# Optimization experiments

Measured on AMD Instinct MI355X. Metric: run time of the kernel, lower is better.

The kernel has to match this reference:

```python
import jax, jax.numpy as jnp
import numpy as np

V, H, L, B, T = 128, 1024, 2, 64, 512

def setup_inputs() -> dict:
    key = jax.random.key(0)
    ks = jax.random.split(key, 6)
    idx = jax.random.randint(ks[0], (B, T), 0, V, dtype=jnp.int32)
    embed = jax.random.normal(ks[1], (V, H), dtype=jnp.float32) * 0.02
    Wx = jax.random.normal(ks[2], (L, H, 4 * H), dtype=jnp.float32) * (1.0 / np.sqrt(H))
    Wh = jax.random.normal(ks[3], (L, H, 4 * H), dtype=jnp.float32) * (1.0 / np.sqrt(H))
    b = jnp.zeros((L, 4 * H), dtype=jnp.float32)
    W_out = jax.random.normal(ks[4], (H, V), dtype=jnp.float32) * (1.0 / np.sqrt(H))
    return {"idx": idx, "embed": embed, "Wx": Wx, "Wh": Wh, "b": b, "W_out": W_out}

def reference(idx, embed, Wx, Wh, b, W_out):
    # idx: (B,T) int32; embed: (V,H); Wx,Wh: (L,H,4H); b: (L,4H); W_out: (H,V)
    x = embed[idx]                      # (B,T,H)
    Bv, Tv, Hv = x.shape
    Lv = Wx.shape[0]
    c0 = jnp.zeros((Lv, Bv, Hv), dtype=x.dtype)
    h0 = jnp.zeros((Lv, Bv, Hv), dtype=x.dtype)

    def step(carry, x_t):
        c, h = carry                    # each (L,B,H)
        new_c, new_h = [], []
        h_in = x_t                      # (B,H)
        for i in range(Lv):             # fixed small layer count
            gates = h_in @ Wx[i] + h[i] @ Wh[i] + b[i]   # (B,4H)
            i_g, f_g, g_g, o_g = jnp.split(gates, 4, axis=-1)
            c_new = jax.nn.sigmoid(f_g) * c[i] + jax.nn.sigmoid(i_g) * jnp.tanh(g_g)
            h_new = jax.nn.sigmoid(o_g) * jnp.tanh(c_new)
            new_c.append(c_new)
            new_h.append(h_new)
            h_in = h_new                # eval mode: dropout mask == 1
        return (jnp.stack(new_c), jnp.stack(new_h)), h_in

    _, hs_tm = jax.lax.scan(step, (c0, h0), jnp.swapaxes(x, 0, 1))  # (T,B,H)
    hs = jnp.swapaxes(hs_tm, 0, 1)                                  # (B,T,H)
    return hs @ W_out                                               # (B,T,V)
```

## Files before the change

### kernel.cpp

```cpp
#include <hip/hip_runtime.h>
#include <math.h>

#define Hn 1024
#define Gn 4096
#define Bn 64
#define Tn 512
#define Vn 128
#define NWG 196
#define NPH 515
#define HSLOTB 131072
#define NGRP 7
#define GRPSZ 28

typedef float f32x16 __attribute__((ext_vector_type(16)));
typedef int i32x16 __attribute__((ext_vector_type(16)));
typedef unsigned long long u64;

#define MFMAI8(a, b, c) __builtin_amdgcn_mfma_i32_32x32x16_i8(a, b, c, 0, 0, 0)

#define QSCALE 32256.0f
#define C1K (65536.0f / (QSCALE * QSCALE))
#define C23K (256.0f / (QSCALE * QSCALE))

__device__ __forceinline__ float coh_loadf(const float* p) {
  return __hip_atomic_load(p, __ATOMIC_RELAXED, __HIP_MEMORY_SCOPE_AGENT);
}
__device__ __forceinline__ void coh_storef(float* p, float v) {
  __hip_atomic_store(p, v, __ATOMIC_RELAXED, __HIP_MEMORY_SCOPE_AGENT);
}
__device__ __forceinline__ void coh_storeu(unsigned* p, unsigned v) {
  __hip_atomic_store(p, v, __ATOMIC_RELAXED, __HIP_MEMORY_SCOPE_AGENT);
}
__device__ __forceinline__ u64 coh_loadq(const u64* p) {
  return __hip_atomic_load(p, __ATOMIC_RELAXED, __HIP_MEMORY_SCOPE_AGENT);
}

__device__ __forceinline__ float sigf(float x) {
  float e = exp2f(x * -1.442695040888963f);
  return __fdividef(1.f, 1.f + e);
}
__device__ __forceinline__ float tanh_(float x) {
  x = fminf(fmaxf(x, -15.f), 15.f);
  float e = exp2f(x * -2.885390081777926f);
  return __fdividef(1.f - e, 1.f + e);
}
__device__ __forceinline__ int clampq(int v) {
  return v > 32255 ? 32255 : (v < -32255 ? -32255 : v);
}

__global__ void ew0_kernel(const float* __restrict__ embed, const float* __restrict__ Wx0,
                           const float* __restrict__ bias, float* __restrict__ EW0) {
  int n = blockIdx.x * 256 + threadIdx.x;
  int vb = blockIdx.y * 8;
  float acc[8] = {0, 0, 0, 0, 0, 0, 0, 0};
  for (int k = 0; k < Hn; k++) {
    float w = Wx0[(size_t)k * Gn + n];
#pragma unroll
    for (int i = 0; i < 8; i++)
      acc[i] = fmaf(embed[(vb + i) * Hn + k], w, acc[i]);
  }
  float bb = bias[n];
#pragma unroll
  for (int i = 0; i < 8; i++)
    EW0[(size_t)(vb + i) * Gn + n] = acc[i] + bb;
}

__device__ __forceinline__ void gridbar(unsigned* bar, int p, int b) {
  asm volatile("s_waitcnt vmcnt(0)" ::: "memory");
  __syncthreads();
  if (threadIdx.x == 0) {
    unsigned* gcnt = bar + (b / GRPSZ) * 32;
    unsigned* ccnt = bar + 256;
    unsigned* flag = bar + 288;
    const unsigned tgt = (unsigned)(p + 1);
    unsigned old = __hip_atomic_fetch_add(gcnt, 1u, __ATOMIC_RELAXED, __HIP_MEMORY_SCOPE_AGENT);
    bool released = false;
    if (old == (unsigned)GRPSZ * tgt - 1u) {
      unsigned c = __hip_atomic_fetch_add(ccnt, 1u, __ATOMIC_RELAXED, __HIP_MEMORY_SCOPE_AGENT);
      if (c == (unsigned)NGRP * tgt - 1u) {
        __hip_atomic_store(flag, tgt, __ATOMIC_RELAXED, __HIP_MEMORY_SCOPE_AGENT);
        released = true;
      }
    }
    if (!released) {
      while (__hip_atomic_load(flag, __ATOMIC_RELAXED, __HIP_MEMORY_SCOPE_AGENT) < tgt)
        __builtin_amdgcn_s_sleep(2);
    }
  }
  __syncthreads();
}

__global__ __launch_bounds__(512, 1)
void persist_kernel(const int* __restrict__ idx,
                    const float* __restrict__ Wx, const float* __restrict__ Wh,
                    const float* __restrict__ bias, const float* __restrict__ Wout,
                    const float* __restrict__ EW0,
                    unsigned char* __restrict__ h0f, unsigned char* __restrict__ h1f,
                    float* __restrict__ P, float* __restrict__ out,
                    unsigned* __restrict__ bar) {
  extern __shared__ char smem[];
  unsigned char* bqhi = (unsigned char*)smem;
  unsigned char* bqlo = (unsigned char*)(smem + 65536);
  float* xg = (float*)(smem + 131072);
  float* cb = (float*)(smem + 131072 + 17408);

  const int b = blockIdx.x, tid = threadIdx.x;
  const int wv = tid >> 6, l = tid & 63;
  const int type = (b < 64) ? 0 : (b < 128) ? 1 : (b < 192) ? 2 : 3;
  const int i = b - ((type == 0) ? 0 : (type == 1) ? 64 : (type == 2) ? 128 : 192);
  const int mtv = wv & 1, khv = wv >> 1;
  const int c32 = l & 31, o8 = (l >> 5) * 8;

  const float* Wsrc = (type == 0) ? Wh
                    : (type == 1) ? (Wx + (size_t)Hn * Gn)
                    : (type == 2) ? (Wh + (size_t)Hn * Gn) : Wout;

  {
    float pmax0 = 0.f, pmax1 = 0.f;
    if (type < 3) {
      for (int nt = 0; nt < 2; nt++) {
        int colv = (c32 >> 3) * Hn + 16 * i + nt * 8 + (c32 & 7);
        float pm = 0.f;
        for (int kk = 0; kk < 8; kk++) {
          int ks = wv * 8 + kk;
#pragma unroll
          for (int e = 0; e < 8; e++)
            pm = fmaxf(pm, fabsf(Wsrc[(size_t)(ks * 16 + o8 + e) * Gn + colv]));
        }
        if (nt) pmax1 = pm; else pmax0 = pm;
      }
    } else {
      int colv = 32 * i + c32;
      for (int kk = 0; kk < 8; kk++) {
        int ks = wv * 8 + kk;
#pragma unroll
        for (int e = 0; e < 8; e++)
          pmax0 = fmaxf(pmax0, fabsf(Wout[(size_t)(ks * 16 + o8 + e) * Vn + colv]));
      }
      pmax1 = 1.f;
    }
    int g = wv * 2 + (l >> 5);
    xg[g * 64 + c32] = pmax0;
    xg[g * 64 + 32 + c32] = pmax1;
  }
  __syncthreads();
  if (tid < 64) {
    float s = 1e-20f;
    for (int g = 0; g < 16; g++) s = fmaxf(s, xg[g * 64 + tid]);
    xg[1024 + tid] = s;
  }
  __syncthreads();
  const float sc0 = xg[1024 + c32], sc1 = xg[1024 + 32 + c32];
  const float qs0 = QSCALE / sc0, qs1 = QSCALE / sc1;
  const float c1v0 = sc0 * C1K, c1v1 = sc1 * C1K;
  const float c23v0 = sc0 * C23K, c23v1 = sc1 * C23K;
  __syncthreads();

  {
    const int ntN = (type < 3) ? 2 : 1;
    for (int nt = 0; nt < ntN; nt++) {
      int colv; size_t stride;
      if (type < 3) { colv = (c32 >> 3) * Hn + 16 * i + nt * 8 + (c32 & 7); stride = Gn; }
      else { colv = 32 * i + c32; stride = Vn; }
      float qs = nt ? qs1 : qs0;
      for (int kk = 0; kk < 8; kk++) {
        int ks = wv * 8 + kk;
        u64 hq = 0, lq = 0;
#pragma unroll
        for (int e = 0; e < 8; e++) {
          float w = Wsrc[(size_t)(ks * 16 + o8 + e) * stride + colv];
          int Wi = clampq((int)rintf(w * qs));
          int bh = (Wi + 128) >> 8;
          int bl = Wi - (bh << 8);
          hq |= (u64)(unsigned char)(bh & 0xFF) << (8 * e);
          lq |= (u64)(unsigned char)(bl & 0xFF) << (8 * e);
        }
        size_t off = ((size_t)nt * 64 + ks) * 512 + (size_t)l * 8;
        *(u64*)(bqhi + off) = hq;
        *(u64*)(bqlo + off) = lq;
      }
    }
  }
  for (int q = tid; q < 1024; q += 512) cb[q] = 0.f;
  __syncthreads();

  for (int p = 0; p < NPH; ++p) {
    const int sA = (p + 1) & 1;
    int t; bool active;
    if (type == 0)      { t = p;     active = (t < Tn); }
    else if (type == 1) { t = p - 1; active = (t >= 0 && t < Tn); }
    else if (type == 2) { t = p - 2; active = (t >= 0 && t < Tn); }
    else                { t = p - 3; active = (t >= 0 && t < Tn); }

    if (active) {
      const unsigned char* A = ((type <= 1) ? h0f : h1f) + (size_t)sA * HSLOTB;
      i32x16 p1a = {}, p23a = {}, p1b = {}, p23b = {};
      const int ks0 = khv * 16;
#pragma unroll
      for (int k2 = 0; k2 < 16; ++k2) {
        const int ks = ks0 + k2;
        long ahi = (long)coh_loadq((const u64*)(A + ((size_t)ks * 4 + mtv) * 512 + (size_t)l * 8));
        long alo = (long)coh_loadq((const u64*)(A + ((size_t)ks * 4 + 2 + mtv) * 512 + (size_t)l * 8));
        size_t bo = (size_t)ks * 512 + (size_t)l * 8;
        long bh0 = *(const long*)(bqhi + bo);
        long bl0 = *(const long*)(bqlo + bo);
        p1a = MFMAI8(ahi, bh0, p1a);
        p23a = MFMAI8(ahi, bl0, p23a);
        p23a = MFMAI8(alo, bh0, p23a);
        if (type < 3) {
          long bh1 = *(const long*)(bqhi + bo + 32768);
          long bl1 = *(const long*)(bqlo + bo + 32768);
          p1b = MFMAI8(ahi, bh1, p1b);
          p23b = MFMAI8(ahi, bl1, p23b);
          p23b = MFMAI8(alo, bh1, p23b);
        }
      }
      f32x16 acc0, acc1;
#pragma unroll
      for (int r = 0; r < 16; ++r) {
        acc0[r] = c1v0 * (float)p1a[r] + c23v0 * (float)p23a[r];
        acc1[r] = (type < 3) ? (c1v1 * (float)p1b[r] + c23v1 * (float)p23b[r]) : 0.f;
      }

#pragma unroll
      for (int rd = 1; rd < 4; ++rd) {
        if (khv == rd) {
          float* s0 = xg + (mtv * 2 + 0) * 1024 + l;
          float* s1 = xg + (mtv * 2 + 1) * 1024 + l;
#pragma unroll
          for (int r = 0; r < 16; ++r) { s0[r * 64] = acc0[r]; s1[r * 64] = acc1[r]; }
        }
        __syncthreads();
        if (khv == 0) {
          const float* s0 = xg + (mtv * 2 + 0) * 1024 + l;
          const float* s1 = xg + (mtv * 2 + 1) * 1024 + l;
#pragma unroll
          for (int r = 0; r < 16; ++r) { acc0[r] += s0[r * 64]; acc1[r] += s1[r * 64]; }
        }
        __syncthreads();
      }

      if (type == 1) {
        if (khv == 0) {
          float* pp = P + ((size_t)(t & 1) * 64 + i) * 4096;
#pragma unroll
          for (int r = 0; r < 16; ++r) {
            int row = (r & 3) + 8 * (r >> 2) + 4 * (l >> 5) + 32 * mtv;
            coh_storef(pp + row * 64 + (l & 31), acc0[r]);
            coh_storef(pp + row * 64 + 32 + (l & 31), acc1[r]);
          }
        }
      } else if (type == 3) {
        if (khv == 0) {
#pragma unroll
          for (int r = 0; r < 16; ++r) {
            int row = (r & 3) + 8 * (r >> 2) + 4 * (l >> 5) + 32 * mtv;
            coh_storef(out + ((size_t)row * Tn + t) * Vn + 32 * i + (l & 31), acc0[r]);
          }
        }
      } else {
        if (khv == 0) {
#pragma unroll
          for (int r = 0; r < 16; ++r) {
            int row = (r & 3) + 8 * (r >> 2) + 4 * (l >> 5) + 32 * mtv;
            xg[row * 65 + (l & 31)] = acc0[r];
            xg[row * 65 + 32 + (l & 31)] = acc1[r];
          }
        }
        __syncthreads();
        unsigned char* dst = ((type == 0) ? h0f : h1f) + (size_t)(p & 1) * HSLOTB;
        if (tid < 256) {
          const int jl0 = (tid >> 6) << 2;
          const int r = tid & 63;
          const int ntc = jl0 >> 3;
          unsigned hiw = 0, low = 0;
          const int vIdx = (type == 0) ? idx[r * Tn + t] : 0;
#pragma unroll
          for (int q = 0; q < 4; ++q) {
            int jl = jl0 + q;
            int j = 16 * i + jl;
            int jo = jl & 7;
            float gi_ = xg[r * 65 + ntc * 32 + jo];
            float gf_ = xg[r * 65 + ntc * 32 + 8 + jo];
            float gg_ = xg[r * 65 + ntc * 32 + 16 + jo];
            float go_ = xg[r * 65 + ntc * 32 + 24 + jo];
            if (type == 0) {
              const float* er = EW0 + (size_t)vIdx * Gn + j;
              gi_ += coh_loadf(er);
              gf_ += coh_loadf(er + Hn);
              gg_ += coh_loadf(er + 2 * Hn);
              go_ += coh_loadf(er + 3 * Hn);
            } else {
              const float* pr = P + ((size_t)(t & 1) * 64 + i) * 4096 + r * 64 + ntc * 32;
              gi_ += coh_loadf(pr + jo) + coh_loadf(bias + Gn + j);
              gf_ += coh_loadf(pr + 8 + jo) + coh_loadf(bias + Gn + Hn + j);
              gg_ += coh_loadf(pr + 16 + jo) + coh_loadf(bias + Gn + 2 * Hn + j);
              go_ += coh_loadf(pr + 24 + jo) + coh_loadf(bias + Gn + 3 * Hn + j);
            }
            float c_ = cb[jl * 64 + r];
            float cn = sigf(gf_) * c_ + sigf(gi_) * tanh_(gg_);
            float hn = sigf(go_) * tanh_(cn);
            cb[jl * 64 + r] = cn;
            int Hq = clampq((int)rintf(hn * QSCALE));
            int ah8 = (Hq + 128) >> 8;
            int al8 = Hq - (ah8 << 8);
            hiw |= ((unsigned)(unsigned char)(ah8 & 0xFF)) << (8 * q);
            low |= ((unsigned)(unsigned char)(al8 & 0xFF)) << (8 * q);
          }
          const int lt = (r & 31) | ((jl0 >> 3) << 5);
          const int e0 = jl0 & 7;
          const int mtt = r >> 5;
          size_t offh = ((size_t)i * 4 + mtt) * 512 + (size_t)lt * 8 + e0;
          coh_storeu((unsigned*)(dst + offh), hiw);
          coh_storeu((unsigned*)(dst + offh + 1024), low);
        }
      }
    }
    gridbar(bar, p, b);
  }
}

extern "C" void kernel_launch(void* const* d_in, const int* in_sizes, int n_in,
                              void* d_out, int out_size, void* d_ws, size_t ws_size,
                              hipStream_t stream) {
  const int* idx = (const int*)d_in[0];
  const float* embed = (const float*)d_in[1];
  const float* Wx = (const float*)d_in[2];
  const float* Wh = (const float*)d_in[3];
  const float* bias = (const float*)d_in[4];
  const float* Wout = (const float*)d_in[5];
  float* out = (float*)d_out;

  float* EW0 = (float*)d_ws;
  unsigned char* h0f = (unsigned char*)(EW0 + 524288);
  unsigned char* h1f = h0f + 2 * HSLOTB;
  float* P = (float*)(h1f + 2 * HSLOTB);
  unsigned* bar = (unsigned*)(P + 524288);

  hipMemsetAsync(h0f, 0, (size_t)4 * HSLOTB, stream);
  hipMemsetAsync(bar, 0, 4096, stream);

  ew0_kernel<<<dim3(Gn / 256, Vn / 8), 256, 0, stream>>>(embed, Wx, bias, EW0);

  hipFuncSetAttribute((const void*)persist_kernel,
                      hipFuncAttributeMaxDynamicSharedMemorySize, 152576);

  void* args[] = {(void*)&idx, (void*)&Wx, (void*)&Wh, (void*)&bias, (void*)&Wout,
                  (void*)&EW0, (void*)&h0f, (void*)&h1f,
                  (void*)&P, (void*)&out, (void*)&bar};
  hipLaunchCooperativeKernel((const void*)persist_kernel, dim3(NWG), dim3(512),
                             args, 152576, stream);

  (void)embed; (void)in_sizes; (void)n_in; (void)out_size; (void)ws_size;
}
```

Before: 6.648 ms.

## Replace serial k-split reduction with LDS atomics and spread cell update over all threads

The three-round staged cross-wave reduction, which had six block barriers, becomes one plain LDS write followed by LDS atomicAdd from the other k-split waves, leaving two barriers. The gate pre-activations (embedding projections or the P partials) are now loaded before the MFMA loop so their latency overlaps compute, and layer-1 bias is hoisted out of the time loop. The LSTM cell update now uses all 512 threads with 2 units each instead of 256 threads with 4, and the P and out stores are re-tiled through LDS for coalesced writes. LDS float atomics add contention, and the narrower 16-bit stores mean more store instructions.

After: 14.63 ms. 2.2x slower.

```diff
diff --git a/kernel.cpp b/kernel.cpp
--- a/kernel.cpp
+++ b/kernel.cpp
@@ -28,7 +28,7 @@
 __device__ __forceinline__ void coh_storef(float* p, float v) {
   __hip_atomic_store(p, v, __ATOMIC_RELAXED, __HIP_MEMORY_SCOPE_AGENT);
 }
-__device__ __forceinline__ void coh_storeu(unsigned* p, unsigned v) {
+__device__ __forceinline__ void coh_storeus(unsigned short* p, unsigned short v) {
   __hip_atomic_store(p, v, __ATOMIC_RELAXED, __HIP_MEMORY_SCOPE_AGENT);
 }
 __device__ __forceinline__ u64 coh_loadq(const u64* p) {
@@ -182,6 +182,19 @@
     }
   }
   for (int q = tid; q < 1024; q += 512) cb[q] = 0.f;
+
+  const int jl0 = (tid >> 6) << 1;
+  const int ur = tid & 63;
+  const int ntc = jl0 >> 3;
+  float bb2[8];
+  if (type == 2) {
+#pragma unroll
+    for (int q = 0; q < 2; ++q) {
+      int j = 16 * i + jl0 + q;
+#pragma unroll
+      for (int g = 0; g < 4; ++g) bb2[q * 4 + g] = bias[Gn + g * Hn + j];
+    }
+  }
   __syncthreads();
 
   for (int p = 0; p < NPH; ++p) {
@@ -193,6 +206,24 @@
     else                { t = p - 3; active = (t >= 0 && t < Tn); }
 
     if (active) {
+      float pre[8];
+      if (type == 0) {
+        const int v = idx[ur * Tn + t];
+        const float* er = EW0 + (size_t)v * Gn + 16 * i + jl0;
+#pragma unroll
+        for (int q = 0; q < 2; ++q)
+#pragma unroll
+          for (int g = 0; g < 4; ++g)
+            pre[q * 4 + g] = coh_loadf(er + q + g * Hn);
+      } else if (type == 2) {
+        const float* pr = P + ((size_t)(t & 1) * 64 + i) * 4096 + ur * 64 + ntc * 32;
+#pragma unroll
+        for (int q = 0; q < 2; ++q)
+#pragma unroll
+          for (int g = 0; g < 4; ++g)
+            pre[q * 4 + g] = coh_loadf(pr + g * 8 + ((jl0 & 7) + q));
+      }
+
       const unsigned char* A = ((type <= 1) ? h0f : h1f) + (size_t)sA * HSLOTB;
       i32x16 p1a = {}, p23a = {}, p1b = {}, p23b = {};
       const int ks0 = khv * 16;
@@ -222,98 +253,70 @@
         acc1[r] = (type < 3) ? (c1v1 * (float)p1b[r] + c23v1 * (float)p23b[r]) : 0.f;
       }
 
-#pragma unroll
-      for (int rd = 1; rd < 4; ++rd) {
-        if (khv == rd) {
-          float* s0 = xg + (mtv * 2 + 0) * 1024 + l;
-          float* s1 = xg + (mtv * 2 + 1) * 1024 + l;
-#pragma unroll
-          for (int r = 0; r < 16; ++r) { s0[r * 64] = acc0[r]; s1[r * 64] = acc1[r]; }
-        }
-        __syncthreads();
-        if (khv == 0) {
-          const float* s0 = xg + (mtv * 2 + 0) * 1024 + l;
-          const float* s1 = xg + (mtv * 2 + 1) * 1024 + l;
-#pragma unroll
-          for (int r = 0; r < 16; ++r) { acc0[r] += s0[r * 64]; acc1[r] += s1[r * 64]; }
-        }
-        __syncthreads();
-      }
+      if (khv == 0) {
+#pragma unroll
+        for (int r = 0; r < 16; ++r) {
+          int row = (r & 3) + 8 * (r >> 2) + 4 * (l >> 5) + 32 * mtv;
+          xg[row * 65 + c32] = acc0[r];
+          xg[row * 65 + 32 + c32] = acc1[r];
+        }
+      }
+      __syncthreads();
+      if (khv != 0) {
+#pragma unroll
+        for (int r = 0; r < 16; ++r) {
+          int row = (r & 3) + 8 * (r >> 2) + 4 * (l >> 5) + 32 * mtv;
+          atomicAdd(&xg[row * 65 + c32], acc0[r]);
+          atomicAdd(&xg[row * 65 + 32 + c32], acc1[r]);
+        }
+      }
+      __syncthreads();
 
       if (type == 1) {
-        if (khv == 0) {
-          float* pp = P + ((size_t)(t & 1) * 64 + i) * 4096;
-#pragma unroll
-          for (int r = 0; r < 16; ++r) {
-            int row = (r & 3) + 8 * (r >> 2) + 4 * (l >> 5) + 32 * mtv;
-            coh_storef(pp + row * 64 + (l & 31), acc0[r]);
-            coh_storef(pp + row * 64 + 32 + (l & 31), acc1[r]);
+        float* pp = P + ((size_t)(t & 1) * 64 + i) * 4096;
+#pragma unroll
+        for (int k = 0; k < 8; ++k) {
+          int r = wv * 8 + k;
+          coh_storef(pp + r * 64 + l, xg[r * 65 + l]);
+        }
+      } else if (type == 3) {
+        const int oc = tid & 31, org = tid >> 5;
+#pragma unroll
+        for (int k = 0; k < 4; ++k) {
+          int r = org * 4 + k;
+          coh_storef(out + ((size_t)r * Tn + t) * Vn + 32 * i + oc, xg[r * 65 + oc]);
+        }
+      } else {
+        unsigned char* dst = ((type == 0) ? h0f : h1f) + (size_t)(p & 1) * HSLOTB;
+        unsigned hi2 = 0, lo2 = 0;
+#pragma unroll
+        for (int q = 0; q < 2; ++q) {
+          int jl = jl0 + q;
+          int jo = jl & 7;
+          float gi_ = xg[ur * 65 + ntc * 32 + jo] + pre[q * 4 + 0];
+          float gf_ = xg[ur * 65 + ntc * 32 + 8 + jo] + pre[q * 4 + 1];
+          float gg_ = xg[ur * 65 + ntc * 32 + 16 + jo] + pre[q * 4 + 2];
+          float go_ = xg[ur * 65 + ntc * 32 + 24 + jo] + pre[q * 4 + 3];
+          if (type == 2) {
+            gi_ += bb2[q * 4 + 0]; gf_ += bb2[q * 4 + 1];
+            gg_ += bb2[q * 4 + 2]; go_ += bb2[q * 4 + 3];
           }
-        }
-      } else if (type == 3) {
-        if (khv == 0) {
-#pragma unroll
-          for (int r = 0; r < 16; ++r) {
-            int row = (r & 3) + 8 * (r >> 2) + 4 * (l >> 5) + 32 * mtv;
-            coh_storef(out + ((size_t)row * Tn + t) * Vn + 32 * i + (l & 31), acc0[r]);
-          }
-        }
-      } else {
-        if (khv == 0) {
-#pragma unroll
-          for (int r = 0; r < 16; ++r) {
-            int row = (r & 3) + 8 * (r >> 2) + 4 * (l >> 5) + 32 * mtv;
-            xg[row * 65 + (l & 31)] = acc0[r];
-            xg[row * 65 + 32 + (l & 31)] = acc1[r];
-          }
-        }
-        __syncthreads();
-        unsigned char* dst = ((type == 0) ? h0f : h1f) + (size_t)(p & 1) * HSLOTB;
-        if (tid < 256) {
-          const int jl0 = (tid >> 6) << 2;
-          const int r = tid & 63;
-          const int ntc = jl0 >> 3;
-          unsigned hiw = 0, low = 0;
-          const int vIdx = (type == 0) ? idx[r * Tn + t] : 0;
-#pragma unroll
-          for (int q = 0; q < 4; ++q) {
-            int jl = jl0 + q;
-            int j = 16 * i + jl;
-            int jo = jl & 7;
-            float gi_ = xg[r * 65 + ntc * 32 + jo];
-            float gf_ = xg[r * 65 + ntc * 32 + 8 + jo];
-            float gg_ = xg[r * 65 + ntc * 32 + 16 + jo];
-            float go_ = xg[r * 65 + ntc * 32 + 24 + jo];
-            if (type == 0) {
-              const float* er = EW0 + (size_t)vIdx * Gn + j;
-              gi_ += coh_loadf(er);
-              gf_ += coh_loadf(er + Hn);
-              gg_ += coh_loadf(er + 2 * Hn);
-              go_ += coh_loadf(er + 3 * Hn);
-            } else {
-              const float* pr = P + ((size_t)(t & 1) * 64 + i) * 4096 + r * 64 + ntc * 32;
-              gi_ += coh_loadf(pr + jo) + coh_loadf(bias + Gn + j);
-              gf_ += coh_loadf(pr + 8 + jo) + coh_loadf(bias + Gn + Hn + j);
-              gg_ += coh_loadf(pr + 16 + jo) + coh_loadf(bias + Gn + 2 * Hn + j);
-              go_ += coh_loadf(pr + 24 + jo) + coh_loadf(bias + Gn + 3 * Hn + j);
-            }
-            float c_ = cb[jl * 64 + r];
-            float cn = sigf(gf_) * c_ + sigf(gi_) * tanh_(gg_);
-            float hn = sigf(go_) * tanh_(cn);
-            cb[jl * 64 + r] = cn;
-            int Hq = clampq((int)rintf(hn * QSCALE));
-            int ah8 = (Hq + 128) >> 8;
-            int al8 = Hq - (ah8 << 8);
-            hiw |= ((unsigned)(unsigned char)(ah8 & 0xFF)) << (8 * q);
-            low |= ((unsigned)(unsigned char)(al8 & 0xFF)) << (8 * q);
-          }
-          const int lt = (r & 31) | ((jl0 >> 3) << 5);
-          const int e0 = jl0 & 7;
-          const int mtt = r >> 5;
-          size_t offh = ((size_t)i * 4 + mtt) * 512 + (size_t)lt * 8 + e0;
-          coh_storeu((unsigned*)(dst + offh), hiw);
-          coh_storeu((unsigned*)(dst + offh + 1024), low);
-        }
+          float c_ = cb[jl * 64 + ur];
+          float cn = sigf(gf_) * c_ + sigf(gi_) * tanh_(gg_);
+          float hn = sigf(go_) * tanh_(cn);
+          cb[jl * 64 + ur] = cn;
+          int Hq = clampq((int)rintf(hn * QSCALE));
+          int ah8 = (Hq + 128) >> 8;
+          int al8 = Hq - (ah8 << 8);
+          hi2 |= ((unsigned)(unsigned char)(ah8 & 0xFF)) << (8 * q);
+          lo2 |= ((unsigned)(unsigned char)(al8 & 0xFF)) << (8 * q);
+        }
+        const int lt = (ur & 31) | ((jl0 >> 3) << 5);
+        const int e0 = jl0 & 7;
+        const int mtt = ur >> 5;
+        size_t offh = ((size_t)i * 4 + mtt) * 512 + (size_t)lt * 8 + e0;
+        coh_storeus((unsigned short*)(dst + offh), (unsigned short)hi2);
+        coh_storeus((unsigned short*)(dst + offh + 1024), (unsigned short)lo2);
       }
     }
     gridbar(bar, p, b);
```
